# Kernel optimization log

Hardware: AMD Instinct MI355X
Metric: run time of the kernel (lower is better)

The kernel has to match this reference:

```python
import jax, jax.numpy as jnp
import numpy as np

NUM_HEADS = 8
ATTN_DIM = 512
DIM_HEAD = ATTN_DIM // NUM_HEADS
SCALE = DIM_HEAD ** -0.5
GN_EPS = 1e-5


def setup_inputs() -> dict:
    key = jax.random.key(0)
    k1, k2, k3 = jax.random.split(key, 3)
    B, H, W, C_IN, C_OUT = 8, 32, 32, 256, 256
    x = jax.random.normal(k1, (B, H, W, C_IN), dtype=jnp.float32)
    w_qkv = jax.random.normal(k2, (C_IN, 3 * ATTN_DIM), dtype=jnp.float32) * (C_IN ** -0.5)
    w_out = jax.random.normal(k3, (ATTN_DIM, C_OUT), dtype=jnp.float32) * (ATTN_DIM ** -0.5)
    b_out = jnp.zeros((C_OUT,), dtype=jnp.float32)
    gamma = jnp.ones((C_OUT,), dtype=jnp.float32)
    beta = jnp.zeros((C_OUT,), dtype=jnp.float32)
    return {"x": x, "w_qkv": w_qkv, "w_out": w_out, "b_out": b_out, "gamma": gamma, "beta": beta}


def reference(x, w_qkv, w_out, b_out, gamma, beta):
    B, H, W, _ = x.shape
    N = H * W
    # 1x1 conv QKV projection (no bias)
    qkv = jnp.einsum('bhwc,cd->bhwd', x, w_qkv)
    q, k, v = jnp.split(qkv, 3, axis=-1)
    # NHWC -> (B, heads, dim_head, HW), matching tf transpose+reshape
    def to_heads(t):
        return t.transpose(0, 3, 1, 2).reshape(B, NUM_HEADS, DIM_HEAD, N)
    q = to_heads(q) * SCALE
    k = to_heads(k)
    v = to_heads(v)
    # sim = q^T k over dim_head: (B, heads, N_q, N_k)
    sim = jnp.einsum('bhcn,bhcm->bhnm', q, k)
    attn = jax.nn.softmax(sim, axis=-1)  # includes the max-subtraction of the original
    # out = attn @ v^T: (B, heads, N, dim_head)
    out = jnp.einsum('bhnm,bhcm->bhnc', attn, v)
    # faithful tf.reshape((B,-1,H,W)) then NCHW->NHWC transpose
    out = out.reshape(B, -1, H, W).transpose(0, 2, 3, 1)  # (B, H, W, attn_dim)
    # output 1x1 conv (with bias) + GroupNorm(groups=1): normalize over (H, W, C) per sample
    y = jnp.einsum('bhwc,cd->bhwd', out, w_out) + b_out
    mean = jnp.mean(y, axis=(1, 2, 3), keepdims=True)
    var = jnp.var(y, axis=(1, 2, 3), keepdims=True)
    y = (y - mean) * jax.lax.rsqrt(var + GN_EPS)
    return y * gamma + beta
```

## Files before the change

kernel.cpp:

```cpp
#include <hip/hip_runtime.h>
#include <math.h>

#define NPOS   1024
#define CIN    256
#define DQKV   1536
#define ATTND  512
#define HEADS  8
#define DH     64
#define COUT   256
#define NBATCH 8
#define SCALE  0.125f
#define GN_EPS 1e-5f

typedef __attribute__((ext_vector_type(8))) __bf16 bf16x8;
typedef __attribute__((ext_vector_type(4))) __bf16 bf16x4;
typedef __attribute__((ext_vector_type(4))) float floatx4;
typedef __attribute__((ext_vector_type(8))) unsigned short ushort8;

#define OFF_XB   (0ull)
#define OFF_WT   (4ull*1048576)
#define OFF_WOT  (4ull*1048576 + 786432ull)
#define OFF_QB   (5ull*1048576)
#define OFF_KB   (13ull*1048576)
#define OFF_VB   (21ull*1048576)
#define OFF_VT   (29ull*1048576)
#define OFF_O2TT (45ull*1048576)
#define OFF_ST   (53ull*1048576)

__global__ __launch_bounds__(256) void prep(
    const float* __restrict__ x, const float* __restrict__ w_qkv,
    const float* __restrict__ w_out,
    __bf16* __restrict__ xb, unsigned short* __restrict__ wT,
    unsigned short* __restrict__ woT, float* __restrict__ stats)
{
    const int bid = blockIdx.x;
    const int t = threadIdx.x;
    __shared__ unsigned short tile[64][68];

    if (bid < 1024) {
        if (bid == 0) stats[t] = 0.0f;
        const int i = (bid * 256 + t) * 8;
        float4 a = *(const float4*)&x[i];
        float4 b = *(const float4*)&x[i + 4];
        bf16x8 o;
        o[0] = (__bf16)a.x; o[1] = (__bf16)a.y; o[2] = (__bf16)a.z; o[3] = (__bf16)a.w;
        o[4] = (__bf16)b.x; o[5] = (__bf16)b.y; o[6] = (__bf16)b.z; o[7] = (__bf16)b.w;
        *(bf16x8*)&xb[i] = o;
        return;
    }

    if (bid < 1120) {
        const int idx = bid - 1024;
        const int n0 = (idx >> 2) * 64, k0 = (idx & 3) * 64;
        #pragma unroll
        for (int p = 0; p < 4; ++p) {
            const int row = p * 16 + (t >> 4);
            const int c = (t & 15) * 4;
            float4 a = *(const float4*)&w_qkv[(size_t)(k0 + row) * DQKV + n0 + c];
            float sv[4] = {a.x, a.y, a.z, a.w};
            #pragma unroll
            for (int j = 0; j < 4; ++j) {
                const float sc = (n0 + c + j) < 512 ? SCALE : 1.0f;
                __bf16 hb = (__bf16)(sv[j] * sc);
                tile[row][c + j] = *(unsigned short*)&hb;
            }
        }
        __syncthreads();
        const int nn = t >> 2;
        const int kc = (t & 3) * 16;
        unsigned short tmp[16];
        #pragma unroll
        for (int j = 0; j < 16; ++j) tmp[j] = tile[kc + j][nn];
        *(ushort8*)&wT[(size_t)(n0 + nn) * 256 + k0 + kc]     = *(ushort8*)&tmp[0];
        *(ushort8*)&wT[(size_t)(n0 + nn) * 256 + k0 + kc + 8] = *(ushort8*)&tmp[8];
        return;
    }

    const int idx = bid - 1120;
    const int d0 = (idx & 3) * 64, k0 = (idx >> 2) * 64;
    #pragma unroll
    for (int p = 0; p < 4; ++p) {
        const int row = p * 16 + (t >> 4);
        const int c = (t & 15) * 4;
        float4 a = *(const float4*)&w_out[(size_t)(k0 + row) * COUT + d0 + c];
        float sv[4] = {a.x, a.y, a.z, a.w};
        #pragma unroll
        for (int j = 0; j < 4; ++j) {
            __bf16 hb = (__bf16)sv[j];
            tile[row][c + j] = *(unsigned short*)&hb;
        }
    }
    __syncthreads();
    {
        const int nn = t >> 2;
        const int kc = (t & 3) * 16;
        unsigned short tmp[16];
        #pragma unroll
        for (int j = 0; j < 16; ++j) tmp[j] = tile[kc + j][nn];
        *(ushort8*)&woT[(size_t)(d0 + nn) * 512 + k0 + kc]     = *(ushort8*)&tmp[0];
        *(ushort8*)&woT[(size_t)(d0 + nn) * 512 + k0 + kc + 8] = *(ushort8*)&tmp[8];
    }
}

__global__ __launch_bounds__(256) void qkv_gemm_mfma(
    const __bf16* __restrict__ xb, const __bf16* __restrict__ wT,
    __bf16* __restrict__ qb, __bf16* __restrict__ kb, __bf16* __restrict__ vb)
{
    const int t = threadIdx.x;
    const int w = t >> 6, lane = t & 63;
    const int col = lane & 15, qd = lane >> 4;
    const int wm = w >> 1, wn = w & 1;
    const int m0 = blockIdx.x * 128, n0 = blockIdx.y * 128;

    __shared__ __align__(16) unsigned short As[128][40];
    __shared__ __align__(16) unsigned short Bs[128][40];

    floatx4 zero4 = {0.f, 0.f, 0.f, 0.f};
    floatx4 acc[4][4];
    #pragma unroll
    for (int i = 0; i < 4; ++i)
        #pragma unroll
        for (int j = 0; j < 4; ++j) acc[i][j] = zero4;

    const int lrow = t >> 2, lc8 = (t & 3) * 8;

    ushort8 areg[2], breg[2];
    areg[0] = *(const ushort8*)&xb[(size_t)(m0 + lrow) * 256 + lc8];
    areg[1] = *(const ushort8*)&xb[(size_t)(m0 + lrow + 64) * 256 + lc8];
    breg[0] = *(const ushort8*)&wT[(size_t)(n0 + lrow) * 256 + lc8];
    breg[1] = *(const ushort8*)&wT[(size_t)(n0 + lrow + 64) * 256 + lc8];

    for (int kk = 0; kk < 8; ++kk) {
        __syncthreads();
        *(ushort8*)&As[lrow][lc8]      = areg[0];
        *(ushort8*)&As[lrow + 64][lc8] = areg[1];
        *(ushort8*)&Bs[lrow][lc8]      = breg[0];
        *(ushort8*)&Bs[lrow + 64][lc8] = breg[1];
        __syncthreads();
        const int kn = (kk < 7) ? (kk + 1) * 32 : 0;
        areg[0] = *(const ushort8*)&xb[(size_t)(m0 + lrow) * 256 + kn + lc8];
        areg[1] = *(const ushort8*)&xb[(size_t)(m0 + lrow + 64) * 256 + kn + lc8];
        breg[0] = *(const ushort8*)&wT[(size_t)(n0 + lrow) * 256 + kn + lc8];
        breg[1] = *(const ushort8*)&wT[(size_t)(n0 + lrow + 64) * 256 + kn + lc8];

        bf16x8 wf[4];
        #pragma unroll
        for (int ct = 0; ct < 4; ++ct)
            wf[ct] = *(const bf16x8*)&Bs[wn * 64 + ct * 16 + col][qd * 8];
        #pragma unroll
        for (int st = 0; st < 4; ++st) {
            bf16x8 xf = *(const bf16x8*)&As[wm * 64 + st * 16 + col][qd * 8];
            #pragma unroll
            for (int ct = 0; ct < 4; ++ct)
                acc[ct][st] = __builtin_amdgcn_mfma_f32_16x16x32_bf16(wf[ct], xf, acc[ct][st], 0, 0, 0);
        }
    }

    #pragma unroll
    for (int ct = 0; ct < 4; ++ct) {
        const int cbase = n0 + wn * 64 + ct * 16;
        const int sect = cbase >> 9;
        const int hh = (cbase >> 6) & 7;
        const int dd = (cbase & 63) + qd * 4;
        __bf16* base = (sect == 0) ? qb : ((sect == 1) ? kb : vb);
        #pragma unroll
        for (int st = 0; st < 4; ++st) {
            const int m = m0 + wm * 64 + st * 16 + col;
            const int b_ = m >> 10, n = m & 1023;
            bf16x4 o;
            #pragma unroll
            for (int r = 0; r < 4; ++r) o[r] = (__bf16)acc[ct][st][r];
            *(bf16x4*)&base[(((size_t)b_ * HEADS + hh) * NPOS + n) * DH + dd] = o;
        }
    }
}

__global__ __launch_bounds__(256) void vtrans(
    const unsigned short* __restrict__ v, unsigned short* __restrict__ vT)
{
    const int bid = blockIdx.x;
    const int bh = bid >> 4, n0 = (bid & 15) * 64;
    __shared__ __align__(16) unsigned short tile[64][72];
    const int t = threadIdx.x;
    #pragma unroll
    for (int p = 0; p < 2; ++p) {
        const int idx = p * 256 + t;
        const int row = idx >> 3, c8 = (idx & 7) * 8;
        *(ushort8*)&tile[row][c8] = *(const ushort8*)&v[((size_t)bh * NPOS + n0 + row) * DH + c8];
    }
    __syncthreads();
    #pragma unroll
    for (int p = 0; p < 2; ++p) {
        const int idx = p * 256 + t;
        const int c = idx >> 3, r8 = (idx & 7) * 8;
        unsigned short tmp[8];
        #pragma unroll
        for (int j = 0; j < 8; ++j) tmp[j] = tile[r8 + j][c];
        *(ushort8*)&vT[((size_t)bh * DH + c) * NPOS + n0 + r8] = *(ushort8*)&tmp[0];
    }
}

__global__ __launch_bounds__(256, 4) void attn_mfma(
    const __bf16* __restrict__ qg, const __bf16* __restrict__ kg,
    const __bf16* __restrict__ vTg, __bf16* __restrict__ o2tT)
{
    const int bid = blockIdx.x;
    const int qblk = bid & 15, h = (bid >> 4) & 7, b = bid >> 7;
    const int bh = b * HEADS + h;
    const int t = threadIdx.x;
    const int w = t >> 6, lane = t & 63;
    const int col = lane & 15;
    const int qd = lane >> 4;

    __shared__ __align__(16) unsigned short Ks[64][72];
    __shared__ __align__(16) unsigned short Vts[64][72];
    __shared__ __align__(16) unsigned short ps[4][16][68];

    const __bf16* qptr = qg + ((size_t)bh * NPOS + qblk * 64 + w * 16 + col) * DH;
    const bf16x8 qf0 = *(const bf16x8*)(qptr + qd * 8);
    const bf16x8 qf1 = *(const bf16x8*)(qptr + 32 + qd * 8);

    const unsigned short* kbase  = (const unsigned short*)kg  + (size_t)bh * NPOS * DH;
    const unsigned short* vtbase = (const unsigned short*)vTg + (size_t)bh * DH * NPOS;

    const int r0 = t >> 3, c8 = (t & 7) * 8;

    ushort8 kreg[2], vreg[2];
    kreg[0] = *(const ushort8*)&kbase[(size_t)r0 * DH + c8];
    kreg[1] = *(const ushort8*)&kbase[(size_t)(r0 + 32) * DH + c8];
    vreg[0] = *(const ushort8*)&vtbase[(size_t)r0 * NPOS + c8];
    vreg[1] = *(const ushort8*)&vtbase[(size_t)(r0 + 32) * NPOS + c8];

    floatx4 zero4 = {0.f, 0.f, 0.f, 0.f};
    floatx4 accO[4];
    #pragma unroll
    for (int i = 0; i < 4; ++i) accO[i] = zero4;
    float lsum_acc = 0.0f;

    for (int kt = 0; kt < 16; ++kt) {
        __syncthreads();
        *(ushort8*)&Ks[r0][c8]       = kreg[0];
        *(ushort8*)&Ks[r0 + 32][c8]  = kreg[1];
        *(ushort8*)&Vts[r0][c8]      = vreg[0];
        *(ushort8*)&Vts[r0 + 32][c8] = vreg[1];
        __syncthreads();

        const int ktn = (kt < 15) ? kt + 1 : 15;
        kreg[0] = *(const ushort8*)&kbase[(size_t)(ktn * 64 + r0) * DH + c8];
        kreg[1] = *(const ushort8*)&kbase[(size_t)(ktn * 64 + r0 + 32) * DH + c8];
        vreg[0] = *(const ushort8*)&vtbase[(size_t)r0 * NPOS + ktn * 64 + c8];
        vreg[1] = *(const ushort8*)&vtbase[(size_t)(r0 + 32) * NPOS + ktn * 64 + c8];

        floatx4 accS[4];
        #pragma unroll
        for (int mt = 0; mt < 4; ++mt) accS[mt] = zero4;
        #pragma unroll
        for (int mt = 0; mt < 4; ++mt) {
            bf16x8 kf0 = *(const bf16x8*)&Ks[mt * 16 + col][qd * 8];
            bf16x8 kf1 = *(const bf16x8*)&Ks[mt * 16 + col][32 + qd * 8];
            accS[mt] = __builtin_amdgcn_mfma_f32_16x16x32_bf16(kf0, qf0, accS[mt], 0, 0, 0);
            accS[mt] = __builtin_amdgcn_mfma_f32_16x16x32_bf16(kf1, qf1, accS[mt], 0, 0, 0);
        }

        #pragma unroll
        for (int mt = 0; mt < 4; ++mt) {
            bf16x4 pv;
            #pragma unroll
            for (int r = 0; r < 4; ++r) {
                const float e = __expf(accS[mt][r]);
                lsum_acc += e;
                pv[r] = (__bf16)e;
            }
            *(bf16x4*)&ps[w][col][mt * 16 + qd * 4] = pv;
        }

        const bf16x8 pf0 = *(const bf16x8*)&ps[w][col][qd * 8];
        const bf16x8 pf1 = *(const bf16x8*)&ps[w][col][32 + qd * 8];
        #pragma unroll
        for (int ct = 0; ct < 4; ++ct) {
            bf16x8 vf0 = *(const bf16x8*)&Vts[ct * 16 + col][qd * 8];
            bf16x8 vf1 = *(const bf16x8*)&Vts[ct * 16 + col][32 + qd * 8];
            accO[ct] = __builtin_amdgcn_mfma_f32_16x16x32_bf16(vf0, pf0, accO[ct], 0, 0, 0);
            accO[ct] = __builtin_amdgcn_mfma_f32_16x16x32_bf16(vf1, pf1, accO[ct], 0, 0, 0);
        }
    }

    lsum_acc += __shfl_xor(lsum_acc, 16);
    lsum_acc += __shfl_xor(lsum_acc, 32);
    const float inv_l = 1.0f / lsum_acc;

    unsigned short (*obuf)[4][68] = (unsigned short (*)[4][68])ps;
    __syncthreads();
    #pragma unroll
    for (int ct = 0; ct < 4; ++ct) {
        bf16x4 o;
        #pragma unroll
        for (int r = 0; r < 4; ++r) o[r] = (__bf16)(accO[ct][r] * inv_l);
        *(bf16x4*)&obuf[col][w][ct * 16 + qd * 4] = o;
    }
    __syncthreads();
    const int chbase = h * 64 + qblk * 4;
    #pragma unroll
    for (int i = 0; i < 4; ++i) {
        const int p = i * 256 + t;
        const int pc = p >> 6, cc = p & 63;
        bf16x4 o;
        #pragma unroll
        for (int w4 = 0; w4 < 4; ++w4) {
            unsigned short u = obuf[pc][w4][cc];
            o[w4] = *(__bf16*)&u;
        }
        *(bf16x4*)&o2tT[((size_t)b * NPOS + p) * ATTND + chbase] = o;
    }
}

__global__ __launch_bounds__(256) void out_mfma(
    const __bf16* __restrict__ a, const __bf16* __restrict__ woT,
    const float* __restrict__ b_out, float* __restrict__ y,
    float* __restrict__ stats)
{
    const int t = threadIdx.x;
    const int w = t >> 6, lane = t & 63;
    const int col = lane & 15, qd = lane >> 4;
    const int wm = w >> 1, wn = w & 1;
    const int m0 = blockIdx.x * 64, d0 = blockIdx.y * 64;
    const int b = blockIdx.x >> 4;

    __shared__ __align__(16) unsigned short As[64][72];
    __shared__ __align__(16) unsigned short Bs[64][72];
    __shared__ float reds[4], redq[4];

    floatx4 zero4 = {0.f, 0.f, 0.f, 0.f};
    floatx4 acc[2][2];
    #pragma unroll
    for (int i = 0; i < 2; ++i)
        #pragma unroll
        for (int j = 0; j < 2; ++j) acc[i][j] = zero4;

    const int lrow = t >> 2, lc = (t & 3) * 16;

    for (int k0 = 0; k0 < ATTND; k0 += 64) {
        __syncthreads();
        *(ushort8*)&As[lrow][lc]     = *(const ushort8*)&a[(size_t)(m0 + lrow) * ATTND + k0 + lc];
        *(ushort8*)&As[lrow][lc + 8] = *(const ushort8*)&a[(size_t)(m0 + lrow) * ATTND + k0 + lc + 8];
        *(ushort8*)&Bs[lrow][lc]     = *(const ushort8*)&woT[(size_t)(d0 + lrow) * ATTND + k0 + lc];
        *(ushort8*)&Bs[lrow][lc + 8] = *(const ushort8*)&woT[(size_t)(d0 + lrow) * ATTND + k0 + lc + 8];
        __syncthreads();
        bf16x8 af0[2], af1[2];
        #pragma unroll
        for (int mt = 0; mt < 2; ++mt) {
            af0[mt] = *(const bf16x8*)&As[wm * 32 + mt * 16 + col][qd * 8];
            af1[mt] = *(const bf16x8*)&As[wm * 32 + mt * 16 + col][32 + qd * 8];
        }
        #pragma unroll
        for (int nt = 0; nt < 2; ++nt) {
            bf16x8 bf0 = *(const bf16x8*)&Bs[wn * 32 + nt * 16 + col][qd * 8];
            bf16x8 bf1 = *(const bf16x8*)&Bs[wn * 32 + nt * 16 + col][32 + qd * 8];
            #pragma unroll
            for (int mt = 0; mt < 2; ++mt) {
                acc[mt][nt] = __builtin_amdgcn_mfma_f32_16x16x32_bf16(af0[mt], bf0, acc[mt][nt], 0, 0, 0);
                acc[mt][nt] = __builtin_amdgcn_mfma_f32_16x16x32_bf16(af1[mt], bf1, acc[mt][nt], 0, 0, 0);
            }
        }
    }

    float bias_n[2];
    #pragma unroll
    for (int nt = 0; nt < 2; ++nt) bias_n[nt] = b_out[d0 + wn * 32 + nt * 16 + col];

    float bsum = 0.0f, bsq = 0.0f;
    #pragma unroll
    for (int mt = 0; mt < 2; ++mt) {
        #pragma unroll
        for (int r = 0; r < 4; ++r) {
            const int m = m0 + wm * 32 + mt * 16 + qd * 4 + r;
            const int p = m & 1023;
            #pragma unroll
            for (int nt = 0; nt < 2; ++nt) {
                const int d = d0 + wn * 32 + nt * 16 + col;
                const float v = acc[mt][nt][r] + bias_n[nt];
                y[((size_t)b * NPOS + p) * COUT + d] = v;
                bsum += v;
                bsq  += v * v;
            }
        }
    }
    #pragma unroll
    for (int off = 1; off < 64; off <<= 1) {
        bsum += __shfl_xor(bsum, off);
        bsq  += __shfl_xor(bsq, off);
    }
    if (lane == 0) { reds[w] = bsum; redq[w] = bsq; }
    __syncthreads();
    if (t == 0) {
        atomicAdd(&stats[b * 16],       reds[0] + reds[1] + reds[2] + reds[3]);
        atomicAdd(&stats[128 + b * 16], redq[0] + redq[1] + redq[2] + redq[3]);
    }
}

__global__ __launch_bounds__(256) void gn_finalize(
    float* __restrict__ y, const float* __restrict__ stats,
    const float* __restrict__ gamma, const float* __restrict__ beta)
{
    const int idx = blockIdx.x * 256 + threadIdx.x;
    const int e = idx * 4;
    const int b_ = e >> 18;
    const int d = e & (COUT - 1);
    const float invn = 1.0f / (float)(NPOS * COUT);
    const float mean = stats[b_ * 16] * invn;
    const float var  = stats[128 + b_ * 16] * invn - mean * mean;
    const float rsig = rsqrtf(var + GN_EPS);
    float4 vv = *(float4*)&y[e];
    const float4 g  = *(const float4*)&gamma[d];
    const float4 bt = *(const float4*)&beta[d];
    vv.x = (vv.x - mean) * rsig * g.x + bt.x;
    vv.y = (vv.y - mean) * rsig * g.y + bt.y;
    vv.z = (vv.z - mean) * rsig * g.z + bt.z;
    vv.w = (vv.w - mean) * rsig * g.w + bt.w;
    *(float4*)&y[e] = vv;
}

extern "C" void kernel_launch(void* const* d_in, const int* in_sizes, int n_in,
                              void* d_out, int out_size, void* d_ws, size_t ws_size,
                              hipStream_t stream)
{
    const float* x     = (const float*)d_in[0];
    const float* w_qkv = (const float*)d_in[1];
    const float* w_out = (const float*)d_in[2];
    const float* b_out = (const float*)d_in[3];
    const float* gamma = (const float*)d_in[4];
    const float* beta  = (const float*)d_in[5];
    float* out = (float*)d_out;
    char* ws = (char*)d_ws;

    __bf16* xb  = (__bf16*)(ws + OFF_XB);
    unsigned short* wT  = (unsigned short*)(ws + OFF_WT);
    unsigned short* woT = (unsigned short*)(ws + OFF_WOT);
    __bf16* qb  = (__bf16*)(ws + OFF_QB);
    __bf16* kb  = (__bf16*)(ws + OFF_KB);
    __bf16* vb  = (__bf16*)(ws + OFF_VB);
    unsigned short* vT  = (unsigned short*)(ws + OFF_VT);
    __bf16* o2tT = (__bf16*)(ws + OFF_O2TT);
    float* stats = (float*)(ws + OFF_ST);

    prep         <<<dim3(1152),   256, 0, stream>>>(x, w_qkv, w_out, xb, wT, woT, stats);
    qkv_gemm_mfma<<<dim3(64, 12), 256, 0, stream>>>(xb, (const __bf16*)wT, qb, kb, vb);
    vtrans       <<<dim3(1024),   256, 0, stream>>>((const unsigned short*)vb, vT);
    attn_mfma    <<<dim3(1024),   256, 0, stream>>>(qb, kb, (const __bf16*)vT, o2tT);
    out_mfma     <<<dim3(128, 4), 256, 0, stream>>>(o2tT, (const __bf16*)woT, b_out, out, stats);
    gn_finalize  <<<dim3(2048),   256, 0, stream>>>(out, stats, gamma, beta);
}
```

Measured before the change: 142.3 us.

## Fuse V transpose into QKV GEMM epilogue and double query rows per attention block

The QKV GEMM epilogue now writes V directly in the transposed (dh, N) layout using scalar bf16 stores, which removes the separate vtrans kernel and its extra read/write pass. The attention kernel now handles 128 query rows per block (two 16-row sub-tiles per wave), so each K/V tile staged in LDS is reused across twice as many queries. The grid is halved and launch bounds drop to 2 blocks per CU. The trade-offs are uncoalesced 2-byte strided stores for V in the GEMM and higher register pressure and lower parallelism in attention.

```diff
diff --git a/kernel.cpp b/kernel.cpp
--- a/kernel.cpp
+++ b/kernel.cpp
@@ -22,7 +22,6 @@
 #define OFF_WOT  (4ull*1048576 + 786432ull)
 #define OFF_QB   (5ull*1048576)
 #define OFF_KB   (13ull*1048576)
-#define OFF_VB   (21ull*1048576)
 #define OFF_VT   (29ull*1048576)
 #define OFF_O2TT (45ull*1048576)
 #define OFF_ST   (53ull*1048576)
@@ -104,7 +103,7 @@
 
 __global__ __launch_bounds__(256) void qkv_gemm_mfma(
     const __bf16* __restrict__ xb, const __bf16* __restrict__ wT,
-    __bf16* __restrict__ qb, __bf16* __restrict__ kb, __bf16* __restrict__ vb)
+    __bf16* __restrict__ qb, __bf16* __restrict__ kb, __bf16* __restrict__ vT)
 {
     const int t = threadIdx.x;
     const int w = t >> 6, lane = t & 63;
@@ -162,50 +161,37 @@
         const int sect = cbase >> 9;
         const int hh = (cbase >> 6) & 7;
         const int dd = (cbase & 63) + qd * 4;
-        __bf16* base = (sect == 0) ? qb : ((sect == 1) ? kb : vb);
-        #pragma unroll
-        for (int st = 0; st < 4; ++st) {
-            const int m = m0 + wm * 64 + st * 16 + col;
-            const int b_ = m >> 10, n = m & 1023;
-            bf16x4 o;
-            #pragma unroll
-            for (int r = 0; r < 4; ++r) o[r] = (__bf16)acc[ct][st][r];
-            *(bf16x4*)&base[(((size_t)b_ * HEADS + hh) * NPOS + n) * DH + dd] = o;
-        }
-    }
-}
-
-__global__ __launch_bounds__(256) void vtrans(
-    const unsigned short* __restrict__ v, unsigned short* __restrict__ vT)
-{
-    const int bid = blockIdx.x;
-    const int bh = bid >> 4, n0 = (bid & 15) * 64;
-    __shared__ __align__(16) unsigned short tile[64][72];
-    const int t = threadIdx.x;
-    #pragma unroll
-    for (int p = 0; p < 2; ++p) {
-        const int idx = p * 256 + t;
-        const int row = idx >> 3, c8 = (idx & 7) * 8;
-        *(ushort8*)&tile[row][c8] = *(const ushort8*)&v[((size_t)bh * NPOS + n0 + row) * DH + c8];
-    }
-    __syncthreads();
-    #pragma unroll
-    for (int p = 0; p < 2; ++p) {
-        const int idx = p * 256 + t;
-        const int c = idx >> 3, r8 = (idx & 7) * 8;
-        unsigned short tmp[8];
-        #pragma unroll
-        for (int j = 0; j < 8; ++j) tmp[j] = tile[r8 + j][c];
-        *(ushort8*)&vT[((size_t)bh * DH + c) * NPOS + n0 + r8] = *(ushort8*)&tmp[0];
-    }
-}
-
-__global__ __launch_bounds__(256, 4) void attn_mfma(
+        if (sect < 2) {
+            __bf16* base = (sect == 0) ? qb : kb;
+            #pragma unroll
+            for (int st = 0; st < 4; ++st) {
+                const int m = m0 + wm * 64 + st * 16 + col;
+                const int b_ = m >> 10, n = m & 1023;
+                bf16x4 o;
+                #pragma unroll
+                for (int r = 0; r < 4; ++r) o[r] = (__bf16)acc[ct][st][r];
+                *(bf16x4*)&base[(((size_t)b_ * HEADS + hh) * NPOS + n) * DH + dd] = o;
+            }
+        } else {
+            #pragma unroll
+            for (int st = 0; st < 4; ++st) {
+                const int m = m0 + wm * 64 + st * 16 + col;
+                const int b_ = m >> 10, n = m & 1023;
+                const size_t rowbase = ((size_t)(b_ * HEADS + hh) * DH + dd) * NPOS + n;
+                #pragma unroll
+                for (int r = 0; r < 4; ++r)
+                    vT[rowbase + (size_t)r * NPOS] = (__bf16)acc[ct][st][r];
+            }
+        }
+    }
+}
+
+__global__ __launch_bounds__(256, 2) void attn_mfma(
     const __bf16* __restrict__ qg, const __bf16* __restrict__ kg,
     const __bf16* __restrict__ vTg, __bf16* __restrict__ o2tT)
 {
     const int bid = blockIdx.x;
-    const int qblk = bid & 15, h = (bid >> 4) & 7, b = bid >> 7;
+    const int qblk = bid & 7, h = (bid >> 3) & 7, b = bid >> 6;
     const int bh = b * HEADS + h;
     const int t = threadIdx.x;
     const int w = t >> 6, lane = t & 63;
@@ -214,11 +200,15 @@
 
     __shared__ __align__(16) unsigned short Ks[64][72];
     __shared__ __align__(16) unsigned short Vts[64][72];
-    __shared__ __align__(16) unsigned short ps[4][16][68];
-
-    const __bf16* qptr = qg + ((size_t)bh * NPOS + qblk * 64 + w * 16 + col) * DH;
-    const bf16x8 qf0 = *(const bf16x8*)(qptr + qd * 8);
-    const bf16x8 qf1 = *(const bf16x8*)(qptr + 32 + qd * 8);
+    __shared__ __align__(16) unsigned short ps[4][32][68];
+
+    bf16x8 qf0[2], qf1[2];
+    #pragma unroll
+    for (int s = 0; s < 2; ++s) {
+        const __bf16* qptr = qg + ((size_t)bh * NPOS + qblk * 128 + s * 64 + w * 16 + col) * DH;
+        qf0[s] = *(const bf16x8*)(qptr + qd * 8);
+        qf1[s] = *(const bf16x8*)(qptr + 32 + qd * 8);
+    }
 
     const unsigned short* kbase  = (const unsigned short*)kg  + (size_t)bh * NPOS * DH;
     const unsigned short* vtbase = (const unsigned short*)vTg + (size_t)bh * DH * NPOS;
@@ -232,10 +222,12 @@
     vreg[1] = *(const ushort8*)&vtbase[(size_t)(r0 + 32) * NPOS + c8];
 
     floatx4 zero4 = {0.f, 0.f, 0.f, 0.f};
-    floatx4 accO[4];
-    #pragma unroll
-    for (int i = 0; i < 4; ++i) accO[i] = zero4;
-    float lsum_acc = 0.0f;
+    floatx4 accO[2][4];
+    #pragma unroll
+    for (int s = 0; s < 2; ++s)
+        #pragma unroll
+        for (int i = 0; i < 4; ++i) accO[s][i] = zero4;
+    float lsum_acc[2] = {0.0f, 0.0f};
 
     for (int kt = 0; kt < 16; ++kt) {
         __syncthreads();
@@ -251,66 +243,84 @@
         vreg[0] = *(const ushort8*)&vtbase[(size_t)r0 * NPOS + ktn * 64 + c8];
         vreg[1] = *(const ushort8*)&vtbase[(size_t)(r0 + 32) * NPOS + ktn * 64 + c8];
 
-        floatx4 accS[4];
-        #pragma unroll
-        for (int mt = 0; mt < 4; ++mt) accS[mt] = zero4;
+        floatx4 accS[2][4];
         #pragma unroll
         for (int mt = 0; mt < 4; ++mt) {
             bf16x8 kf0 = *(const bf16x8*)&Ks[mt * 16 + col][qd * 8];
             bf16x8 kf1 = *(const bf16x8*)&Ks[mt * 16 + col][32 + qd * 8];
-            accS[mt] = __builtin_amdgcn_mfma_f32_16x16x32_bf16(kf0, qf0, accS[mt], 0, 0, 0);
-            accS[mt] = __builtin_amdgcn_mfma_f32_16x16x32_bf16(kf1, qf1, accS[mt], 0, 0, 0);
-        }
-
-        #pragma unroll
-        for (int mt = 0; mt < 4; ++mt) {
-            bf16x4 pv;
-            #pragma unroll
-            for (int r = 0; r < 4; ++r) {
-                const float e = __expf(accS[mt][r]);
-                lsum_acc += e;
-                pv[r] = (__bf16)e;
-            }
-            *(bf16x4*)&ps[w][col][mt * 16 + qd * 4] = pv;
-        }
-
-        const bf16x8 pf0 = *(const bf16x8*)&ps[w][col][qd * 8];
-        const bf16x8 pf1 = *(const bf16x8*)&ps[w][col][32 + qd * 8];
+            #pragma unroll
+            for (int s = 0; s < 2; ++s) {
+                accS[s][mt] = __builtin_amdgcn_mfma_f32_16x16x32_bf16(kf0, qf0[s], zero4, 0, 0, 0);
+                accS[s][mt] = __builtin_amdgcn_mfma_f32_16x16x32_bf16(kf1, qf1[s], accS[s][mt], 0, 0, 0);
+            }
+        }
+
+        #pragma unroll
+        for (int s = 0; s < 2; ++s)
+            #pragma unroll
+            for (int mt = 0; mt < 4; ++mt) {
+                bf16x4 pv;
+                #pragma unroll
+                for (int r = 0; r < 4; ++r) {
+                    const float e = __expf(accS[s][mt][r]);
+                    lsum_acc[s] += e;
+                    pv[r] = (__bf16)e;
+                }
+                *(bf16x4*)&ps[w][s * 16 + col][mt * 16 + qd * 4] = pv;
+            }
+
+        bf16x8 pf0[2], pf1[2];
+        #pragma unroll
+        for (int s = 0; s < 2; ++s) {
+            pf0[s] = *(const bf16x8*)&ps[w][s * 16 + col][qd * 8];
+            pf1[s] = *(const bf16x8*)&ps[w][s * 16 + col][32 + qd * 8];
+        }
+
         #pragma unroll
         for (int ct = 0; ct < 4; ++ct) {
             bf16x8 vf0 = *(const bf16x8*)&Vts[ct * 16 + col][qd * 8];
             bf16x8 vf1 = *(const bf16x8*)&Vts[ct * 16 + col][32 + qd * 8];
-            accO[ct] = __builtin_amdgcn_mfma_f32_16x16x32_bf16(vf0, pf0, accO[ct], 0, 0, 0);
-            accO[ct] = __builtin_amdgcn_mfma_f32_16x16x32_bf16(vf1, pf1, accO[ct], 0, 0, 0);
-        }
-    }
-
-    lsum_acc += __shfl_xor(lsum_acc, 16);
-    lsum_acc += __shfl_xor(lsum_acc, 32);
-    const float inv_l = 1.0f / lsum_acc;
-
-    unsigned short (*obuf)[4][68] = (unsigned short (*)[4][68])ps;
+            #pragma unroll
+            for (int s = 0; s < 2; ++s) {
+                accO[s][ct] = __builtin_amdgcn_mfma_f32_16x16x32_bf16(vf0, pf0[s], accO[s][ct], 0, 0, 0);
+                accO[s][ct] = __builtin_amdgcn_mfma_f32_16x16x32_bf16(vf1, pf1[s], accO[s][ct], 0, 0, 0);
+            }
+        }
+    }
+
+    float inv_l[2];
+    #pragma unroll
+    for (int s = 0; s < 2; ++s) {
+        float l = lsum_acc[s];
+        l += __shfl_xor(l, 16);
+        l += __shfl_xor(l, 32);
+        inv_l[s] = 1.0f / l;
+    }
+
+    unsigned short (*obuf)[8][68] = (unsigned short (*)[8][68])ps;
     __syncthreads();
     #pragma unroll
-    for (int ct = 0; ct < 4; ++ct) {
-        bf16x4 o;
-        #pragma unroll
-        for (int r = 0; r < 4; ++r) o[r] = (__bf16)(accO[ct][r] * inv_l);
-        *(bf16x4*)&obuf[col][w][ct * 16 + qd * 4] = o;
-    }
+    for (int s = 0; s < 2; ++s)
+        #pragma unroll
+        for (int ct = 0; ct < 4; ++ct) {
+            bf16x4 o;
+            #pragma unroll
+            for (int r = 0; r < 4; ++r) o[r] = (__bf16)(accO[s][ct][r] * inv_l[s]);
+            *(bf16x4*)&obuf[col][s * 4 + w][ct * 16 + qd * 4] = o;
+        }
     __syncthreads();
-    const int chbase = h * 64 + qblk * 4;
+    const int chbase = h * 64 + qblk * 8;
     #pragma unroll
     for (int i = 0; i < 4; ++i) {
         const int p = i * 256 + t;
         const int pc = p >> 6, cc = p & 63;
-        bf16x4 o;
-        #pragma unroll
-        for (int w4 = 0; w4 < 4; ++w4) {
-            unsigned short u = obuf[pc][w4][cc];
-            o[w4] = *(__bf16*)&u;
-        }
-        *(bf16x4*)&o2tT[((size_t)b * NPOS + p) * ATTND + chbase] = o;
+        bf16x8 o;
+        #pragma unroll
+        for (int j = 0; j < 8; ++j) {
+            unsigned short u = obuf[pc][j][cc];
+            o[j] = *(__bf16*)&u;
+        }
+        *(bf16x8*)&o2tT[((size_t)b * NPOS + p) * ATTND + chbase] = o;
     }
 }
 
@@ -438,15 +448,13 @@
     unsigned short* woT = (unsigned short*)(ws + OFF_WOT);
     __bf16* qb  = (__bf16*)(ws + OFF_QB);
     __bf16* kb  = (__bf16*)(ws + OFF_KB);
-    __bf16* vb  = (__bf16*)(ws + OFF_VB);
-    unsigned short* vT  = (unsigned short*)(ws + OFF_VT);
+    __bf16* vT  = (__bf16*)(ws + OFF_VT);
     __bf16* o2tT = (__bf16*)(ws + OFF_O2TT);
     float* stats = (float*)(ws + OFF_ST);
 
     prep         <<<dim3(1152),   256, 0, stream>>>(x, w_qkv, w_out, xb, wT, woT, stats);
-    qkv_gemm_mfma<<<dim3(64, 12), 256, 0, stream>>>(xb, (const __bf16*)wT, qb, kb, vb);
-    vtrans       <<<dim3(1024),   256, 0, stream>>>((const unsigned short*)vb, vT);
-    attn_mfma    <<<dim3(1024),   256, 0, stream>>>(qb, kb, (const __bf16*)vT, o2tT);
+    qkv_gemm_mfma<<<dim3(64, 12), 256, 0, stream>>>(xb, (const __bf16*)wT, qb, kb, vT);
+    attn_mfma    <<<dim3(512),    256, 0, stream>>>(qb, kb, vT, o2tT);
     out_mfma     <<<dim3(128, 4), 256, 0, stream>>>(o2tT, (const __bf16*)woT, b_out, out, stats);
     gn_finalize  <<<dim3(2048),   256, 0, stream>>>(out, stats, gamma, beta);
 }
```

Result: faster. 130.7 us (-8.2%).
